# Kernel tuning notes

Hardware: AMD Instinct MI355X
Metric: run time of the kernel (lower is better)

Reference implementation:

```python
import jax, jax.numpy as jnp
import numpy as np


def setup_inputs() -> dict:
    key = jax.random.key(0)
    B, N, M, D = 8, 256, 16, 256
    embeddings = jax.random.normal(key, (B, N, M, D), dtype=jnp.float32)
    w = jnp.asarray(10.0, dtype=jnp.float32)
    b = jnp.asarray(-5.0, dtype=jnp.float32)
    return {"embeddings": embeddings, "w": w, "b": b}


def reference(embeddings, w, b):
    # embeddings: [B, N, M, D]
    B, N, M, D = embeddings.shape
    centroids = jnp.mean(embeddings, axis=2)  # [B, N, D]

    # Cross similarities: S[b,j,i,k] = w * <e_{bji}, c_{bk}> + b
    S = w * jnp.einsum('bjid,bkd->bjik', embeddings, centroids) + b  # [B,N,M,N]

    # Own-centroid case (j == k): leave-one-out centroid
    # <e, (M*c_j - e)/(M-1)> = (M*<e,c_j> - ||e||^2) / (M-1)
    dot_own = jnp.einsum('bjid,bjd->bji', embeddings, centroids)     # [B,N,M]
    sq_norm = jnp.sum(embeddings * embeddings, axis=-1)              # [B,N,M]
    S_self = w * (M * dot_own - sq_norm) / (M - 1) + b               # [B,N,M]

    # Place S_self on the k == j diagonal
    eye = jnp.eye(N, dtype=bool)[None, :, None, :]                   # [1,N,1,N]
    S = jnp.where(eye, S_self[..., None], S)

    # loss = sum log sum_k exp(S) - sum_{j==k} S
    loss = jnp.sum(jax.nn.logsumexp(S, axis=-1)) - jnp.sum(S_self)
    return loss
```

## Files before the change

### kernel.cpp

```cpp
#include <hip/hip_runtime.h>

constexpr int B = 8, N = 256, M = 16, D = 256;

typedef short bf16x8 __attribute__((ext_vector_type(8)));
typedef float f32x4 __attribute__((ext_vector_type(4)));

__device__ __forceinline__ unsigned short f2bf(float x) {
  unsigned u = __float_as_uint(x);
  u = (u + 0x7FFFu + ((u >> 16) & 1u)) >> 16;
  return (unsigned short)u;
}
__device__ __forceinline__ uint4 packbf8(const float* f) {
  uint4 u;
  u.x = (unsigned)f2bf(f[0]) | ((unsigned)f2bf(f[1]) << 16);
  u.y = (unsigned)f2bf(f[2]) | ((unsigned)f2bf(f[3]) << 16);
  u.z = (unsigned)f2bf(f[4]) | ((unsigned)f2bf(f[5]) << 16);
  u.w = (unsigned)f2bf(f[6]) | ((unsigned)f2bf(f[7]) << 16);
  return u;
}


__global__ __launch_bounds__(256) void k_prep(const float* __restrict__ e,
                                              uint4* __restrict__ EbfA,
                                              uint4* __restrict__ Cbf,
                                              float* __restrict__ SQ,
                                              float* __restrict__ out) {
  const int blk = blockIdx.x;
  const int b = blk >> 8, j = blk & 255;
  const int t = threadIdx.x;
  const int w = t >> 6, l = t & 63;
  const int m = l & 15, q = l >> 4;
  const float* base = e + (size_t)blk * (M * D);

  float sqp = 0.f;
  __shared__ float sqred[4][16];

#pragma unroll
  for (int kk = 0; kk < 2; ++kk) {
    const int kc = w * 2 + kk;
    const float* src = base + m * D + kc * 32 + q * 8;
    float f[8];
#pragma unroll
    for (int x = 0; x < 4; ++x) f[x] = ((const float4*)src)->x, f[x] = src[x];
#pragma unroll
    for (int x = 0; x < 8; ++x) f[x] = src[x];
    EbfA[(size_t)(blk * 8 + kc) * 64 + l] = packbf8(f);
#pragma unroll
    for (int x = 0; x < 8; ++x) sqp = fmaf(f[x], f[x], sqp);
    float cv[8];
#pragma unroll
    for (int x = 0; x < 8; ++x) cv[x] = f[x];
#pragma unroll
    for (int mk = 1; mk < 16; mk <<= 1)
#pragma unroll
      for (int x = 0; x < 8; ++x) cv[x] += __shfl_xor(cv[x], mk, 64);
    if (m == (j & 15)) {
      float cs[8];
#pragma unroll
      for (int x = 0; x < 8; ++x) cs[x] = cv[x] * (1.f / 16.f);
      Cbf[(size_t)((b * 8 + kc) * 16 + (j >> 4)) * 64 + l] = packbf8(cs);
    }
  }
  sqp += __shfl_xor(sqp, 16, 64);
  sqp += __shfl_xor(sqp, 32, 64);
  if (q == 0) sqred[w][m] = sqp;
  __syncthreads();
  if (t < 16) SQ[blk * 16 + t] = sqred[0][t] + sqred[1][t] + sqred[2][t] + sqred[3][t];
  if (blk == 0 && t == 0) out[0] = 0.f;
}

__global__ __launch_bounds__(256) void k_gemm(const uint4* __restrict__ EbfA,
                                              const uint4* __restrict__ Cbf,
                                              const float* __restrict__ SQ,
                                              const float* __restrict__ wp,
                                              const float* __restrict__ bp,
                                              float* __restrict__ out) {
  const int blk = blockIdx.x;
  const int b = blk >> 6, strip = blk & 63;
  const int tid = threadIdx.x;
  const int wid = tid >> 6, lane = tid & 63;
  const int h = wid >> 1, c = wid & 1;
  const int q = lane >> 4, cl_ = lane & 15;

  const uint4* Ab = EbfA + (size_t)((b * 256 + strip * 4 + h * 2) * 8) * 64 + lane;
  const uint4* Bb = Cbf + (size_t)(b * 128 + c * 8) * 64 + lane;

  f32x4 acc[2][8];
#pragma unroll
  for (int rt = 0; rt < 2; ++rt)
#pragma unroll
    for (int nt = 0; nt < 8; ++nt) acc[rt][nt] = (f32x4)0.f;

#pragma unroll 1
  for (int kc = 0; kc < 8; ++kc) {
    uint4 af0 = Ab[kc * 64];
    uint4 af1 = Ab[(8 + kc) * 64];
    uint4 bfr[8];
#pragma unroll
    for (int nt = 0; nt < 8; ++nt) bfr[nt] = Bb[(kc * 16 + nt) * 64];
    bf16x8 a0 = __builtin_bit_cast(bf16x8, af0);
    bf16x8 a1 = __builtin_bit_cast(bf16x8, af1);
#pragma unroll
    for (int nt = 0; nt < 8; ++nt) {
      bf16x8 bv = __builtin_bit_cast(bf16x8, bfr[nt]);
      acc[0][nt] = __builtin_amdgcn_mfma_f32_16x16x32_bf16(a0, bv, acc[0][nt], 0, 0, 0);
      acc[1][nt] = __builtin_amdgcn_mfma_f32_16x16x32_bf16(a1, bv, acc[1][nt], 0, 0, 0);
    }
  }

  const float w = *wp, bias = *bp;
  __shared__ float lmx[2][64];
  __shared__ float lsm[2][64];
  __shared__ float bred[4];
  float ssum = 0.f;

#pragma unroll
  for (int rt = 0; rt < 2; ++rt) {
    const int jr = strip * 4 + h * 2 + rt;
    const bool own = (c == (jr >> 7)) && (cl_ == (jr & 15));
    const int ntd = (jr >> 4) & 7;
    float sq[4];
    if (own) {
#pragma unroll
      for (int reg = 0; reg < 4; ++reg)
        sq[reg] = SQ[b * 4096 + strip * 64 + (h * 2 + rt) * 16 + q * 4 + reg];
    }
#pragma unroll
    for (int nt = 0; nt < 8; ++nt)
#pragma unroll
      for (int reg = 0; reg < 4; ++reg) {
        const float raw = acc[rt][nt][reg];
        float sv = fmaf(w, raw, bias);
        if (own && nt == ntd) {
          sv = fmaf(w * (1.f / 15.f), 16.f * raw - sq[reg], bias);
          ssum += sv;
        }
        acc[rt][nt][reg] = sv;
      }
#pragma unroll
    for (int reg = 0; reg < 4; ++reg) {
      float mx = acc[rt][0][reg];
#pragma unroll
      for (int nt = 1; nt < 8; ++nt) mx = fmaxf(mx, acc[rt][nt][reg]);
#pragma unroll
      for (int mk = 1; mk < 16; mk <<= 1) mx = fmaxf(mx, __shfl_xor(mx, mk, 64));
      if (cl_ == 0) lmx[c][(h * 2 + rt) * 16 + q * 4 + reg] = mx;
    }
  }
  __syncthreads();

#pragma unroll
  for (int rt = 0; rt < 2; ++rt)
#pragma unroll
    for (int reg = 0; reg < 4; ++reg) {
      const int Rl = (h * 2 + rt) * 16 + q * 4 + reg;
      const float mx = fmaxf(lmx[0][Rl], lmx[1][Rl]);
      float se = 0.f;
#pragma unroll
      for (int nt = 0; nt < 8; ++nt) se += __expf(acc[rt][nt][reg] - mx);
#pragma unroll
      for (int mk = 1; mk < 16; mk <<= 1) se += __shfl_xor(se, mk, 64);
      if (cl_ == 0) lsm[c][Rl] = se;
    }
  __syncthreads();

  float part = -ssum;
  if (c == 0 && cl_ == 0) {
#pragma unroll
    for (int rt = 0; rt < 2; ++rt)
#pragma unroll
      for (int reg = 0; reg < 4; ++reg) {
        const int Rl = (h * 2 + rt) * 16 + q * 4 + reg;
        const float mx = fmaxf(lmx[0][Rl], lmx[1][Rl]);
        part += mx + __logf(lsm[0][Rl] + lsm[1][Rl]);
      }
  }
#pragma unroll
  for (int mk = 1; mk < 64; mk <<= 1) part += __shfl_xor(part, mk, 64);
  if (lane == 0) bred[wid] = part;
  __syncthreads();
  if (tid == 0) atomicAdd(out, bred[0] + bred[1] + bred[2] + bred[3]);
}

extern "C" void kernel_launch(void* const* d_in, const int* in_sizes, int n_in,
                              void* d_out, int out_size, void* d_ws, size_t ws_size,
                              hipStream_t stream) {
  const float* e = (const float*)d_in[0];
  const float* wp = (const float*)d_in[1];
  const float* bp = (const float*)d_in[2];
  float* out = (float*)d_out;
  char* ws = (char*)d_ws;
  uint4* EbfA = (uint4*)ws;
  uint4* Cbf = (uint4*)(ws + (size_t)16 * 1024 * 1024);
  float* SQ = (float*)(ws + (size_t)17 * 1024 * 1024);

  k_prep<<<B * N, 256, 0, stream>>>(e, EbfA, Cbf, SQ, out);
  k_gemm<<<B * 64, 256, 0, stream>>>(EbfA, Cbf, SQ, wp, bp, out);
}
```

Before: 97.02 us.

## Fuse bf16 conversion and squared norms into GEMM, drop packed embedding buffer

The prep kernel now computes only the centroids, using a column-sum over M and shared memory, and no longer writes a bf16 copy of the embeddings or the squared norms. The GEMM kernel reads fp32 embeddings directly, converts them to bf16 in registers, and accumulates squared norms on the fly, then distributes them with shuffles. This removes a full write and re-read of the bf16 embedding buffer (about 16 MB) and the SQ buffer. In exchange the GEMM kernel reads twice the bytes per A fragment and does the conversion work inside its main loop.

```diff
diff --git a/kernel.cpp b/kernel.cpp
--- a/kernel.cpp
+++ b/kernel.cpp
@@ -21,57 +21,30 @@
 
 
 __global__ __launch_bounds__(256) void k_prep(const float* __restrict__ e,
-                                              uint4* __restrict__ EbfA,
                                               uint4* __restrict__ Cbf,
-                                              float* __restrict__ SQ,
                                               float* __restrict__ out) {
   const int blk = blockIdx.x;
   const int b = blk >> 8, j = blk & 255;
   const int t = threadIdx.x;
-  const int w = t >> 6, l = t & 63;
-  const int m = l & 15, q = l >> 4;
   const float* base = e + (size_t)blk * (M * D);
-
-  float sqp = 0.f;
-  __shared__ float sqred[4][16];
-
+  float s = 0.f;
 #pragma unroll
-  for (int kk = 0; kk < 2; ++kk) {
-    const int kc = w * 2 + kk;
-    const float* src = base + m * D + kc * 32 + q * 8;
+  for (int i = 0; i < M; ++i) s += base[i * D + t];
+  __shared__ float cl[D];
+  cl[t] = s * (1.f / 16.f);
+  __syncthreads();
+  if (t < 32) {
+    const int kc = t >> 2, qq = t & 3;
     float f[8];
 #pragma unroll
-    for (int x = 0; x < 4; ++x) f[x] = ((const float4*)src)->x, f[x] = src[x];
-#pragma unroll
-    for (int x = 0; x < 8; ++x) f[x] = src[x];
-    EbfA[(size_t)(blk * 8 + kc) * 64 + l] = packbf8(f);
-#pragma unroll
-    for (int x = 0; x < 8; ++x) sqp = fmaf(f[x], f[x], sqp);
-    float cv[8];
-#pragma unroll
-    for (int x = 0; x < 8; ++x) cv[x] = f[x];
-#pragma unroll
-    for (int mk = 1; mk < 16; mk <<= 1)
-#pragma unroll
-      for (int x = 0; x < 8; ++x) cv[x] += __shfl_xor(cv[x], mk, 64);
-    if (m == (j & 15)) {
-      float cs[8];
-#pragma unroll
-      for (int x = 0; x < 8; ++x) cs[x] = cv[x] * (1.f / 16.f);
-      Cbf[(size_t)((b * 8 + kc) * 16 + (j >> 4)) * 64 + l] = packbf8(cs);
-    }
+    for (int x = 0; x < 8; ++x) f[x] = cl[kc * 32 + qq * 8 + x];
+    Cbf[(size_t)((b * 8 + kc) * 16 + (j >> 4)) * 64 + qq * 16 + (j & 15)] = packbf8(f);
   }
-  sqp += __shfl_xor(sqp, 16, 64);
-  sqp += __shfl_xor(sqp, 32, 64);
-  if (q == 0) sqred[w][m] = sqp;
-  __syncthreads();
-  if (t < 16) SQ[blk * 16 + t] = sqred[0][t] + sqred[1][t] + sqred[2][t] + sqred[3][t];
   if (blk == 0 && t == 0) out[0] = 0.f;
 }
 
-__global__ __launch_bounds__(256) void k_gemm(const uint4* __restrict__ EbfA,
+__global__ __launch_bounds__(256) void k_gemm(const float* __restrict__ e,
                                               const uint4* __restrict__ Cbf,
-                                              const float* __restrict__ SQ,
                                               const float* __restrict__ wp,
                                               const float* __restrict__ bp,
                                               float* __restrict__ out) {
@@ -80,9 +53,10 @@
   const int tid = threadIdx.x;
   const int wid = tid >> 6, lane = tid & 63;
   const int h = wid >> 1, c = wid & 1;
-  const int q = lane >> 4, cl_ = lane & 15;
+  const int q = lane >> 4, m = lane & 15;
 
-  const uint4* Ab = EbfA + (size_t)((b * 256 + strip * 4 + h * 2) * 8) * 64 + lane;
+  const float* Abase =
+      e + (size_t)b * (N * M * D) + (size_t)((strip * 4 + h * 2) * 16 + m) * D + q * 8;
   const uint4* Bb = Cbf + (size_t)(b * 128 + c * 8) * 64 + lane;
 
   f32x4 acc[2][8];
@@ -90,23 +64,45 @@
   for (int rt = 0; rt < 2; ++rt)
 #pragma unroll
     for (int nt = 0; nt < 8; ++nt) acc[rt][nt] = (f32x4)0.f;
+  float sqp[2] = {0.f, 0.f};
 
 #pragma unroll 1
   for (int kc = 0; kc < 8; ++kc) {
-    uint4 af0 = Ab[kc * 64];
-    uint4 af1 = Ab[(8 + kc) * 64];
+    float fa[2][8];
+#pragma unroll
+    for (int rt = 0; rt < 2; ++rt) {
+      const float4 lo = *(const float4*)(Abase + (size_t)rt * 16 * D + kc * 32);
+      const float4 hi = *(const float4*)(Abase + (size_t)rt * 16 * D + kc * 32 + 4);
+      fa[rt][0] = lo.x; fa[rt][1] = lo.y; fa[rt][2] = lo.z; fa[rt][3] = lo.w;
+      fa[rt][4] = hi.x; fa[rt][5] = hi.y; fa[rt][6] = hi.z; fa[rt][7] = hi.w;
+#pragma unroll
+      for (int x = 0; x < 8; ++x) sqp[rt] = fmaf(fa[rt][x], fa[rt][x], sqp[rt]);
+    }
+    uint4 a0 = packbf8(fa[0]);
+    uint4 a1 = packbf8(fa[1]);
     uint4 bfr[8];
 #pragma unroll
     for (int nt = 0; nt < 8; ++nt) bfr[nt] = Bb[(kc * 16 + nt) * 64];
-    bf16x8 a0 = __builtin_bit_cast(bf16x8, af0);
-    bf16x8 a1 = __builtin_bit_cast(bf16x8, af1);
+    bf16x8 av0 = __builtin_bit_cast(bf16x8, a0);
+    bf16x8 av1 = __builtin_bit_cast(bf16x8, a1);
 #pragma unroll
     for (int nt = 0; nt < 8; ++nt) {
       bf16x8 bv = __builtin_bit_cast(bf16x8, bfr[nt]);
-      acc[0][nt] = __builtin_amdgcn_mfma_f32_16x16x32_bf16(a0, bv, acc[0][nt], 0, 0, 0);
-      acc[1][nt] = __builtin_amdgcn_mfma_f32_16x16x32_bf16(a1, bv, acc[1][nt], 0, 0, 0);
+      acc[0][nt] = __builtin_amdgcn_mfma_f32_16x16x32_bf16(av0, bv, acc[0][nt], 0, 0, 0);
+      acc[1][nt] = __builtin_amdgcn_mfma_f32_16x16x32_bf16(av1, bv, acc[1][nt], 0, 0, 0);
     }
   }
+
+#pragma unroll
+  for (int rt = 0; rt < 2; ++rt) {
+    sqp[rt] += __shfl_xor(sqp[rt], 16, 64);
+    sqp[rt] += __shfl_xor(sqp[rt], 32, 64);
+  }
+  float sqv[2][4];
+#pragma unroll
+  for (int rt = 0; rt < 2; ++rt)
+#pragma unroll
+    for (int reg = 0; reg < 4; ++reg) sqv[rt][reg] = __shfl(sqp[rt], q * 4 + reg, 64);
 
   const float w = *wp, bias = *bp;
   __shared__ float lmx[2][64];
@@ -117,14 +113,8 @@
 #pragma unroll
   for (int rt = 0; rt < 2; ++rt) {
     const int jr = strip * 4 + h * 2 + rt;
-    const bool own = (c == (jr >> 7)) && (cl_ == (jr & 15));
+    const bool own = (c == (jr >> 7)) && (m == (jr & 15));
     const int ntd = (jr >> 4) & 7;
-    float sq[4];
-    if (own) {
-#pragma unroll
-      for (int reg = 0; reg < 4; ++reg)
-        sq[reg] = SQ[b * 4096 + strip * 64 + (h * 2 + rt) * 16 + q * 4 + reg];
-    }
 #pragma unroll
     for (int nt = 0; nt < 8; ++nt)
 #pragma unroll
@@ -132,7 +122,7 @@
         const float raw = acc[rt][nt][reg];
         float sv = fmaf(w, raw, bias);
         if (own && nt == ntd) {
-          sv = fmaf(w * (1.f / 15.f), 16.f * raw - sq[reg], bias);
+          sv = fmaf(w * (1.f / 15.f), 16.f * raw - sqv[rt][reg], bias);
           ssum += sv;
         }
         acc[rt][nt][reg] = sv;
@@ -144,7 +134,7 @@
       for (int nt = 1; nt < 8; ++nt) mx = fmaxf(mx, acc[rt][nt][reg]);
 #pragma unroll
       for (int mk = 1; mk < 16; mk <<= 1) mx = fmaxf(mx, __shfl_xor(mx, mk, 64));
-      if (cl_ == 0) lmx[c][(h * 2 + rt) * 16 + q * 4 + reg] = mx;
+      if (m == 0) lmx[c][(h * 2 + rt) * 16 + q * 4 + reg] = mx;
     }
   }
   __syncthreads();
@@ -160,12 +150,12 @@
       for (int nt = 0; nt < 8; ++nt) se += __expf(acc[rt][nt][reg] - mx);
 #pragma unroll
       for (int mk = 1; mk < 16; mk <<= 1) se += __shfl_xor(se, mk, 64);
-      if (cl_ == 0) lsm[c][Rl] = se;
+      if (m == 0) lsm[c][Rl] = se;
     }
   __syncthreads();
 
   float part = -ssum;
-  if (c == 0 && cl_ == 0) {
+  if (c == 0 && m == 0) {
 #pragma unroll
     for (int rt = 0; rt < 2; ++rt)
 #pragma unroll
@@ -189,11 +179,8 @@
   const float* wp = (const float*)d_in[1];
   const float* bp = (const float*)d_in[2];
   float* out = (float*)d_out;
-  char* ws = (char*)d_ws;
-  uint4* EbfA = (uint4*)ws;
-  uint4* Cbf = (uint4*)(ws + (size_t)16 * 1024 * 1024);
-  float* SQ = (float*)(ws + (size_t)17 * 1024 * 1024);
+  uint4* Cbf = (uint4*)d_ws;
 
-  k_prep<<<B * N, 256, 0, stream>>>(e, EbfA, Cbf, SQ, out);
-  k_gemm<<<B * 64, 256, 0, stream>>>(EbfA, Cbf, SQ, wp, bp, out);
+  k_prep<<<B * N, 256, 0, stream>>>(e, Cbf, out);
+  k_gemm<<<B * 64, 256, 0, stream>>>(e, Cbf, wp, bp, out);
 }
```

Result: no change. 98.66 us (+1.7%).

## Coalesce prep loads via LDS staging and prefetch A fragments in GEMM loop

Applied to the files above, without the earlier changes.

The prep kernel now loads each embedding block with fully coalesced per-thread column reads, computes the centroid by a per-thread column sum, and stages the block in padded shared memory. Bf16 fragments and squared norms are then produced from shared memory, which replaces the strided 8-float global reads and the 15-step shuffle reduction used for the centroid. The GEMM kernel double-buffers the A fragments across k-iterations and hoists the w/bias loads ahead of the loop. The cost is about 16 KB of LDS per block in prep, which may reduce occupancy, plus extra registers for the prefetch.

```diff
diff --git a/kernel.cpp b/kernel.cpp
--- a/kernel.cpp
+++ b/kernel.cpp
@@ -1,6 +1,7 @@
 #include <hip/hip_runtime.h>
 
 constexpr int B = 8, N = 256, M = 16, D = 256;
+constexpr int LTS = 260;
 
 typedef short bf16x8 __attribute__((ext_vector_type(8)));
 typedef float f32x4 __attribute__((ext_vector_type(4)));
@@ -29,41 +30,48 @@
   const int b = blk >> 8, j = blk & 255;
   const int t = threadIdx.x;
   const int w = t >> 6, l = t & 63;
-  const int m = l & 15, q = l >> 4;
+  const int q = l >> 4, m = l & 15;
   const float* base = e + (size_t)blk * (M * D);
 
-  float sqp = 0.f;
+  __shared__ float lt[M * LTS];
+  __shared__ float cl[D];
   __shared__ float sqred[4][16];
 
+  float ev[M];
+  float cs = 0.f;
+#pragma unroll
+  for (int i = 0; i < M; ++i) {
+    ev[i] = base[i * D + t];
+    cs += ev[i];
+  }
+#pragma unroll
+  for (int i = 0; i < M; ++i) lt[i * LTS + t] = ev[i];
+  cl[t] = cs * (1.f / 16.f);
+  __syncthreads();
+
+  float sq = 0.f;
 #pragma unroll
   for (int kk = 0; kk < 2; ++kk) {
-    const int kc = w * 2 + kk;
-    const float* src = base + m * D + kc * 32 + q * 8;
+    const int kc = 2 * w + kk;
+    const float* src = &lt[m * LTS + kc * 32 + q * 8];
     float f[8];
 #pragma unroll
-    for (int x = 0; x < 4; ++x) f[x] = ((const float4*)src)->x, f[x] = src[x];
-#pragma unroll
     for (int x = 0; x < 8; ++x) f[x] = src[x];
+#pragma unroll
+    for (int x = 0; x < 8; ++x) sq = fmaf(f[x], f[x], sq);
     EbfA[(size_t)(blk * 8 + kc) * 64 + l] = packbf8(f);
-#pragma unroll
-    for (int x = 0; x < 8; ++x) sqp = fmaf(f[x], f[x], sqp);
-    float cv[8];
-#pragma unroll
-    for (int x = 0; x < 8; ++x) cv[x] = f[x];
-#pragma unroll
-    for (int mk = 1; mk < 16; mk <<= 1)
-#pragma unroll
-      for (int x = 0; x < 8; ++x) cv[x] += __shfl_xor(cv[x], mk, 64);
-    if (m == (j & 15)) {
-      float cs[8];
-#pragma unroll
-      for (int x = 0; x < 8; ++x) cs[x] = cv[x] * (1.f / 16.f);
-      Cbf[(size_t)((b * 8 + kc) * 16 + (j >> 4)) * 64 + l] = packbf8(cs);
-    }
-  }
-  sqp += __shfl_xor(sqp, 16, 64);
-  sqp += __shfl_xor(sqp, 32, 64);
-  if (q == 0) sqred[w][m] = sqp;
+  }
+  sq += __shfl_xor(sq, 16, 64);
+  sq += __shfl_xor(sq, 32, 64);
+  if (q == 0) sqred[w][m] = sq;
+
+  if (t < 32) {
+    const int kc = t >> 2, qq = t & 3;
+    float f[8];
+#pragma unroll
+    for (int x = 0; x < 8; ++x) f[x] = cl[kc * 32 + qq * 8 + x];
+    Cbf[(size_t)((b * 8 + kc) * 16 + (j >> 4)) * 64 + qq * 16 + (j & 15)] = packbf8(f);
+  }
   __syncthreads();
   if (t < 16) SQ[blk * 16 + t] = sqred[0][t] + sqred[1][t] + sqred[2][t] + sqred[3][t];
   if (blk == 0 && t == 0) out[0] = 0.f;
@@ -80,7 +88,8 @@
   const int tid = threadIdx.x;
   const int wid = tid >> 6, lane = tid & 63;
   const int h = wid >> 1, c = wid & 1;
-  const int q = lane >> 4, cl_ = lane & 15;
+  const int q = lane >> 4, m = lane & 15;
+  const float w = *wp, bias = *bp;
 
   const uint4* Ab = EbfA + (size_t)((b * 256 + strip * 4 + h * 2) * 8) * 64 + lane;
   const uint4* Bb = Cbf + (size_t)(b * 128 + c * 8) * 64 + lane;
@@ -91,24 +100,28 @@
 #pragma unroll
     for (int nt = 0; nt < 8; ++nt) acc[rt][nt] = (f32x4)0.f;
 
+  uint4 aC0 = Ab[0], aC1 = Ab[8 * 64];
 #pragma unroll 1
   for (int kc = 0; kc < 8; ++kc) {
-    uint4 af0 = Ab[kc * 64];
-    uint4 af1 = Ab[(8 + kc) * 64];
+    uint4 aN0, aN1;
+    if (kc < 7) {
+      aN0 = Ab[(kc + 1) * 64];
+      aN1 = Ab[(8 + kc + 1) * 64];
+    }
     uint4 bfr[8];
 #pragma unroll
     for (int nt = 0; nt < 8; ++nt) bfr[nt] = Bb[(kc * 16 + nt) * 64];
-    bf16x8 a0 = __builtin_bit_cast(bf16x8, af0);
-    bf16x8 a1 = __builtin_bit_cast(bf16x8, af1);
+    const bf16x8 av0 = __builtin_bit_cast(bf16x8, aC0);
+    const bf16x8 av1 = __builtin_bit_cast(bf16x8, aC1);
 #pragma unroll
     for (int nt = 0; nt < 8; ++nt) {
-      bf16x8 bv = __builtin_bit_cast(bf16x8, bfr[nt]);
-      acc[0][nt] = __builtin_amdgcn_mfma_f32_16x16x32_bf16(a0, bv, acc[0][nt], 0, 0, 0);
-      acc[1][nt] = __builtin_amdgcn_mfma_f32_16x16x32_bf16(a1, bv, acc[1][nt], 0, 0, 0);
-    }
-  }
-
-  const float w = *wp, bias = *bp;
+      const bf16x8 bv = __builtin_bit_cast(bf16x8, bfr[nt]);
+      acc[0][nt] = __builtin_amdgcn_mfma_f32_16x16x32_bf16(av0, bv, acc[0][nt], 0, 0, 0);
+      acc[1][nt] = __builtin_amdgcn_mfma_f32_16x16x32_bf16(av1, bv, acc[1][nt], 0, 0, 0);
+    }
+    if (kc < 7) { aC0 = aN0; aC1 = aN1; }
+  }
+
   __shared__ float lmx[2][64];
   __shared__ float lsm[2][64];
   __shared__ float bred[4];
@@ -117,13 +130,13 @@
 #pragma unroll
   for (int rt = 0; rt < 2; ++rt) {
     const int jr = strip * 4 + h * 2 + rt;
-    const bool own = (c == (jr >> 7)) && (cl_ == (jr & 15));
+    const bool own = (c == (jr >> 7)) && (m == (jr & 15));
     const int ntd = (jr >> 4) & 7;
-    float sq[4];
+    float sqv[4];
     if (own) {
 #pragma unroll
       for (int reg = 0; reg < 4; ++reg)
-        sq[reg] = SQ[b * 4096 + strip * 64 + (h * 2 + rt) * 16 + q * 4 + reg];
+        sqv[reg] = SQ[b * 4096 + jr * 16 + q * 4 + reg];
     }
 #pragma unroll
     for (int nt = 0; nt < 8; ++nt)
@@ -132,7 +145,7 @@
         const float raw = acc[rt][nt][reg];
         float sv = fmaf(w, raw, bias);
         if (own && nt == ntd) {
-          sv = fmaf(w * (1.f / 15.f), 16.f * raw - sq[reg], bias);
+          sv = fmaf(w * (1.f / 15.f), 16.f * raw - sqv[reg], bias);
           ssum += sv;
         }
         acc[rt][nt][reg] = sv;
@@ -144,7 +157,7 @@
       for (int nt = 1; nt < 8; ++nt) mx = fmaxf(mx, acc[rt][nt][reg]);
 #pragma unroll
       for (int mk = 1; mk < 16; mk <<= 1) mx = fmaxf(mx, __shfl_xor(mx, mk, 64));
-      if (cl_ == 0) lmx[c][(h * 2 + rt) * 16 + q * 4 + reg] = mx;
+      if (m == 0) lmx[c][(h * 2 + rt) * 16 + q * 4 + reg] = mx;
     }
   }
   __syncthreads();
@@ -160,12 +173,12 @@
       for (int nt = 0; nt < 8; ++nt) se += __expf(acc[rt][nt][reg] - mx);
 #pragma unroll
       for (int mk = 1; mk < 16; mk <<= 1) se += __shfl_xor(se, mk, 64);
-      if (cl_ == 0) lsm[c][Rl] = se;
+      if (m == 0) lsm[c][Rl] = se;
     }
   __syncthreads();
 
   float part = -ssum;
-  if (c == 0 && cl_ == 0) {
+  if (c == 0 && m == 0) {
 #pragma unroll
     for (int rt = 0; rt < 2; ++rt)
 #pragma unroll
```

After: 100.5 us. +3.6%, slower.
